# Kernel tuning notes

Measured on AMD Instinct MI355X. Metric: run time of the kernel, lower is better.

The kernel has to match this reference:

```python
import jax, jax.numpy as jnp
import numpy as np

# dims
N, M, L, E = 50000, 1024, 3, 200000      # tgt nodes, src nodes, subtokens/node, edges
HID, EMB, VOCAB = 512, 256, 512
N_SLT, N_SRT = 4, 5                       # SLT edge types (messages), SRT edge types (output head)
W_SCALE = 0.02


def setup_inputs() -> dict:
    key = jax.random.key(0)
    ks = jax.random.split(key, 20)
    inp = {
        "tgt_x": jax.random.randint(ks[0], (N, L), 0, VOCAB),
        "x": jax.random.normal(ks[1], (M, HID), jnp.float32),
        "tgt_edge_index": jax.random.randint(ks[2], (2, E), 0, N),
        "tgt_edge_type": jax.random.randint(ks[3], (E,), 0, N_SLT),
        "embed_table": jax.random.normal(ks[4], (VOCAB, EMB), jnp.float32) * W_SCALE,
        # GCN layer 1 (called twice in the original forward) and layer 3 params
        "W_h1": jax.random.normal(ks[5], (EMB, EMB), jnp.float32) * W_SCALE,
        "W_rel1": jax.random.normal(ks[6], (N_SLT, EMB, EMB), jnp.float32) * W_SCALE,
        "W_src1": jax.random.normal(ks[7], (HID, EMB), jnp.float32) * W_SCALE,
        "W_h3": jax.random.normal(ks[8], (EMB, EMB), jnp.float32) * W_SCALE,
        "W_rel3": jax.random.normal(ks[9], (N_SLT, EMB, EMB), jnp.float32) * W_SCALE,
        "W_src3": jax.random.normal(ks[10], (HID, EMB), jnp.float32) * W_SCALE,
        # output heads
        "Wz": jax.random.normal(ks[11], (EMB, VOCAB), jnp.float32) * W_SCALE,
        "bz": jnp.zeros((VOCAB,), jnp.float32),
        "Wg": jax.random.normal(ks[12], (2 * EMB, N_SRT), jnp.float32) * W_SCALE,
        "bg": jnp.zeros((N_SRT,), jnp.float32),
    }
    return inp


def _gcn_layer(x_src, h, edge_index, edge_type, W_h, W_rel, W_src):
    """Relational GCN decoder layer with cross-attention to encoder nodes."""
    k = x_src @ W_src                                   # [M, EMB]
    attn = jax.nn.softmax(h @ k.T / jnp.sqrt(jnp.float32(EMB)), axis=1)  # [N, M]
    ctx = attn @ k                                      # [N, EMB]
    # per-edge-type transform first ([N, T, EMB]), then gather per edge
    h_t = jnp.einsum('nd,tdf->ntf', h, W_rel)           # [N, N_SLT, EMB]
    src, tgt = edge_index[0], edge_index[1]
    msg = h_t[src, edge_type]                           # [E, EMB] gather
    agg = jax.ops.segment_sum(msg, tgt, num_segments=h.shape[0])  # [N, EMB]
    return jax.nn.relu(h @ W_h + agg + ctx)


def reference(tgt_x, x, tgt_edge_index, tgt_edge_type, embed_table,
              W_h1, W_rel1, W_src1, W_h3, W_rel3, W_src3, Wz, bz, Wg, bg):
    # embedding + reduction over subtokens
    h = embed_table[tgt_x].sum(axis=1)                  # [N, EMB]
    # original code calls gcn1 twice, then gcn3 (gcn2 unused in training path)
    h = _gcn_layer(x, h, tgt_edge_index, tgt_edge_type, W_h1, W_rel1, W_src1)
    h = _gcn_layer(x, h, tgt_edge_index, tgt_edge_type, W_h1, W_rel1, W_src1)
    h = _gcn_layer(x, h, tgt_edge_index, tgt_edge_type, W_h3, W_rel3, W_src3)
    # node head
    node_pred = jax.nn.log_softmax(h @ Wz + bz, axis=1)  # [N, VOCAB]
    # edge head: gather [2,E,EMB] -> permute -> [E, 2*EMB]
    ef = h[tgt_edge_index]                               # [2, E, EMB]
    ef = jnp.transpose(ef, (1, 0, 2)).reshape(E, 2 * EMB)
    edge_pred = jax.nn.log_softmax(ef @ Wg + bg, axis=1)  # [E, N_SRT]
    return node_pred, edge_pred
```

## Files before the change

### kernel.cpp

```cpp
#include <hip/hip_runtime.h>
#include <hip/hip_bf16.h>
#include <cstdint>

#define N_NODES 50000
#define M_SRC   1024
#define E_EDGES 200000
#define EMB     256
#define HIDN    512
#define VOCABSZ 512

typedef __attribute__((ext_vector_type(8))) short bf16x8;
typedef __attribute__((ext_vector_type(4))) short bf16x4;
typedef __attribute__((ext_vector_type(4))) float f32x4;

__device__ inline short f2b(float f) {
    __hip_bfloat16 b = __float2bfloat16(f);
    return *reinterpret_cast<short*>(&b);
}
__device__ inline float b2f(short s) {
    __hip_bfloat16 b = *reinterpret_cast<__hip_bfloat16*>(&s);
    return __bfloat162float(b);
}

__device__ inline void gload16(const void* g, void* l) {
    __builtin_amdgcn_global_load_lds(
        (const __attribute__((address_space(1))) unsigned int*)g,
        (__attribute__((address_space(3))) unsigned int*)l,
        16, 0, 0);
}

__device__ inline void tr_read2(unsigned addr, bf16x4& lo, bf16x4& hi) {
    asm volatile("ds_read_b64_tr_b16 %0, %2\n\tds_read_b64_tr_b16 %1, %2 offset:512"
                 : "=&v"(lo), "=&v"(hi) : "v"(addr));
}

__global__ void embed_kernel(const int* __restrict__ tgt_x,
                             const float* __restrict__ table,
                             short* __restrict__ h)
{
    int n = blockIdx.x, d = threadIdx.x;
    const int* tx = tgt_x + (size_t)n * 3;
    float s = table[(size_t)tx[0] * EMB + d]
            + table[(size_t)tx[1] * EMB + d]
            + table[(size_t)tx[2] * EMB + d];
    h[(size_t)n * EMB + d] = f2b(s);
}

__global__ void convert_kernel(const float* __restrict__ in, short* __restrict__ out, int n)
{
    int i = blockIdx.x * 256 + threadIdx.x;
    if (i * 4 < n) {
        float4 v = *(const float4*)&in[i * 4];
        short4 o;
        o.x = f2b(v.x); o.y = f2b(v.y); o.z = f2b(v.z); o.w = f2b(v.w);
        *(short4*)&out[i * 4] = o;
    }
}

template<typename TIN>
__global__ void transpose_kernel(const TIN* __restrict__ in, short* __restrict__ out, int R, int C)
{
    __shared__ float t[32][33];
    int tx = threadIdx.x & 31, ty = threadIdx.x >> 5;
    int r0 = blockIdx.y * 32, c0 = blockIdx.x * 32;
#pragma unroll
    for (int i = 0; i < 4; i++) {
        int r = ty + i * 8;
        TIN v = in[(size_t)(r0 + r) * C + c0 + tx];
        if constexpr (sizeof(TIN) == 4) t[r][tx] = v;
        else                            t[r][tx] = b2f(v);
    }
    __syncthreads();
#pragma unroll
    for (int i = 0; i < 4; i++) {
        int r = ty + i * 8;
        out[(size_t)(c0 + r) * R + r0 + tx] = f2b(t[tx][r]);
    }
}

__global__ void transposeW_kernel(const float* __restrict__ Wh1, const float* __restrict__ Wh3,
                                  const float* __restrict__ Wr1, const float* __restrict__ Wr3,
                                  short* __restrict__ WhT1, short* __restrict__ WhT3,
                                  short* __restrict__ WrT1, short* __restrict__ WrT3)
{
    __shared__ float t[32][33];
    const int z = blockIdx.z;
    const float* in; short* outp;
    if (z == 0)      { in = Wh1;                               outp = WhT1; }
    else if (z == 1) { in = Wh3;                               outp = WhT3; }
    else if (z < 6)  { in = Wr1 + (size_t)(z - 2) * EMB * EMB; outp = WrT1 + (size_t)(z - 2) * EMB * EMB; }
    else             { in = Wr3 + (size_t)(z - 6) * EMB * EMB; outp = WrT3 + (size_t)(z - 6) * EMB * EMB; }
    int tx = threadIdx.x & 31, ty = threadIdx.x >> 5;
    int r0 = blockIdx.y * 32, c0 = blockIdx.x * 32;
#pragma unroll
    for (int i = 0; i < 4; i++) {
        int r = ty + i * 8;
        t[r][tx] = in[(size_t)(r0 + r) * EMB + c0 + tx];
    }
    __syncthreads();
#pragma unroll
    for (int i = 0; i < 4; i++) {
        int r = ty + i * 8;
        outp[(size_t)(c0 + r) * EMB + r0 + tx] = f2b(t[tx][r]);
    }
}

template<int MODE>
__global__ __launch_bounds__(256) void mgemm(
    const short* __restrict__ A, const short* __restrict__ BT,
    void* __restrict__ outp, const float* __restrict__ aux,
    const float* __restrict__ bias, int NR, int K, int J)
{
    __shared__ short As[128 * 40];
    __shared__ short Bs[128 * 40];
    const int tid  = threadIdx.x;
    const int n0   = blockIdx.x * 128;
    const int j0   = blockIdx.y * 128;
    const int lane = tid & 63, wid = tid >> 6;
    const int wr   = wid >> 1, wc = wid & 1;

    f32x4 acc[4][4];
#pragma unroll
    for (int m = 0; m < 4; m++)
#pragma unroll
        for (int n = 0; n < 4; n++) acc[m][n] = (f32x4){0.f, 0.f, 0.f, 0.f};

    for (int kt = 0; kt < K; kt += 32) {
#pragma unroll
        for (int r = 0; r < 2; r++) {
            int idx = tid + r * 256;
            int row = idx >> 2, ko = (idx & 3) * 8;
            int n = n0 + row;
            bf16x8 av = {0, 0, 0, 0, 0, 0, 0, 0};
            if (n < NR) av = *(const bf16x8*)&A[(size_t)n * K + kt + ko];
            *(bf16x8*)&As[row * 40 + ko] = av;
            *(bf16x8*)&Bs[row * 40 + ko] = *(const bf16x8*)&BT[(size_t)(j0 + row) * K + kt + ko];
        }
        __syncthreads();
        bf16x8 af[4], bfr[4];
#pragma unroll
        for (int m = 0; m < 4; m++)
            af[m] = *(const bf16x8*)&As[(wr * 64 + m * 16 + (lane & 15)) * 40 + (lane >> 4) * 8];
#pragma unroll
        for (int n = 0; n < 4; n++)
            bfr[n] = *(const bf16x8*)&Bs[(wc * 64 + n * 16 + (lane & 15)) * 40 + (lane >> 4) * 8];
#pragma unroll
        for (int m = 0; m < 4; m++)
#pragma unroll
            for (int n = 0; n < 4; n++)
                acc[m][n] = __builtin_amdgcn_mfma_f32_16x16x32_bf16(af[m], bfr[n], acc[m][n], 0, 0, 0);
        __syncthreads();
    }

#pragma unroll
    for (int m = 0; m < 4; m++) {
        int rbase = wr * 64 + m * 16 + ((lane >> 4) * 4);
#pragma unroll
        for (int r = 0; r < 4; r++) {
            int n_g = n0 + rbase + r;
            if (n_g >= NR) continue;
#pragma unroll
            for (int nn = 0; nn < 4; nn++) {
                int j_g = j0 + wc * 64 + nn * 16 + (lane & 15);
                float v = acc[m][nn][r];
                if constexpr (MODE == 0) {
                    ((short*)outp)[(size_t)n_g * J + j_g] = f2b(v);
                } else {
                    float a = aux[(size_t)n_g * J + j_g];
                    ((short*)outp)[(size_t)n_g * J + j_g] = f2b(fmaxf(v + a, 0.f));
                }
            }
        }
    }
}

__global__ __launch_bounds__(256, 2) void attn_flash(
    const short* __restrict__ h, const short* __restrict__ kb,
    float* __restrict__ C, int NR)
{
    __shared__ short ks[2][32 * 256];
    __shared__ short Ps[64 * 36];

    const int tid = threadIdx.x;
    const int lane = tid & 63, wv = tid >> 6;
    const int l4 = lane >> 4, l15 = lane & 15;
    const int n0 = blockIdx.x * 64;
    const int hrow = wv * 16 + l15;

    auto LOFF = [](int key, int d8) {
        return (d8 & 1) * 8 + (key & 3) * 16 + ((key >> 3) & 3) * 64
             + ((key >> 2) & 1) * 256 + (d8 >> 1) * 512;
    };
    int keyq[4], d8q[4];
#pragma unroll
    for (int q = 0; q < 4; q++) {
        int ci = wv * 64 + lane + q * 256;
        d8q[q]  = (ci & 1) | ((ci >> 6) << 1);
        keyq[q] = ((ci >> 1) & 3) | (((ci >> 5) & 1) << 2) | (((ci >> 3) & 3) << 3);
    }

    bf16x8 hreg[8];
    {
        int n = n0 + hrow;
        const short* hp = &h[(size_t)(n < NR ? n : 0) * 256 + l4 * 8];
#pragma unroll
        for (int kst = 0; kst < 8; kst++) hreg[kst] = *(const bf16x8*)&hp[kst * 32];
        if (n >= NR) {
#pragma unroll
            for (int kst = 0; kst < 8; kst++) hreg[kst] = (bf16x8){0, 0, 0, 0, 0, 0, 0, 0};
        }
    }

#pragma unroll
    for (int q = 0; q < 4; q++)
        gload16(&kb[(size_t)keyq[q] * 256 + d8q[q] * 8], &ks[0][q * 2048 + wv * 512]);
    __syncthreads();

    const unsigned ksbase = (unsigned)(uintptr_t)&ks[0][0];
    const unsigned trlane = 2u * (unsigned)(l15 + l4 * 64);

    f32x4 oacc[16];
#pragma unroll
    for (int mm = 0; mm < 16; mm++) oacc[mm] = (f32x4){0.f, 0.f, 0.f, 0.f};
    float lsum = 0.f;

    for (int c = 0; c < 32; c++) {
        const int cur = c & 1;
        if (c + 1 < 32) {
            const short* kbn = kb + (size_t)(c + 1) * 32 * 256;
#pragma unroll
            for (int q = 0; q < 4; q++)
                gload16(&kbn[(size_t)keyq[q] * 256 + d8q[q] * 8], &ks[cur ^ 1][q * 2048 + wv * 512]);
        }

        f32x4 sacc[2];
        sacc[0] = (f32x4){0.f, 0.f, 0.f, 0.f};
        sacc[1] = (f32x4){0.f, 0.f, 0.f, 0.f};
        __builtin_amdgcn_s_setprio(1);
#pragma unroll
        for (int kst = 0; kst < 8; kst++) {
#pragma unroll
            for (int m = 0; m < 2; m++) {
                int krow = m * 16 + l15;
                bf16x8 afk = *(const bf16x8*)&ks[cur][LOFF(krow, kst * 4 + l4)];
                sacc[m] = __builtin_amdgcn_mfma_f32_16x16x32_bf16(afk, hreg[kst], sacc[m], 0, 0, 0);
            }
        }
        __builtin_amdgcn_s_setprio(0);
        float psum = 0.f;
#pragma unroll
        for (int m = 0; m < 2; m++) {
            float p0 = __expf(sacc[m][0] * 0.0625f);
            float p1 = __expf(sacc[m][1] * 0.0625f);
            float p2 = __expf(sacc[m][2] * 0.0625f);
            float p3 = __expf(sacc[m][3] * 0.0625f);
            psum += (p0 + p1) + (p2 + p3);
            short4 pk;
            pk.x = f2b(p0); pk.y = f2b(p1); pk.z = f2b(p2); pk.w = f2b(p3);
            *(short4*)&Ps[hrow * 36 + m * 16 + l4 * 4] = pk;
        }
        psum += __shfl_xor(psum, 16);
        psum += __shfl_xor(psum, 32);
        lsum += psum;

        bf16x8 bf2 = *(const bf16x8*)&Ps[(wv * 16 + l15) * 36 + l4 * 8];
        unsigned trb = ksbase + (unsigned)(cur * 16384) + trlane;
#pragma unroll
        for (int g = 0; g < 2; g++) {
            bf16x4 lo[8], hi[8];
#pragma unroll
            for (int q = 0; q < 8; q++)
                tr_read2(trb + (unsigned)((g * 8 + q) * 1024), lo[q], hi[q]);
            asm volatile("s_waitcnt lgkmcnt(0)" ::: "memory");
            __builtin_amdgcn_sched_barrier(0);
            __builtin_amdgcn_s_setprio(1);
#pragma unroll
            for (int q = 0; q < 8; q++) {
                bf16x8 af2;
#pragma unroll
                for (int t2 = 0; t2 < 4; t2++) { af2[t2] = lo[q][t2]; af2[t2 + 4] = hi[q][t2]; }
                oacc[g * 8 + q] = __builtin_amdgcn_mfma_f32_16x16x32_bf16(af2, bf2, oacc[g * 8 + q], 0, 0, 0);
            }
            __builtin_amdgcn_s_setprio(0);
        }

        __syncthreads();
    }

    float li = 1.0f / lsum;
    int hr = n0 + hrow;
    if (hr < NR) {
#pragma unroll
        for (int mm = 0; mm < 16; mm++) {
            float4 v;
            v.x = oacc[mm][0] * li;
            v.y = oacc[mm][1] * li;
            v.z = oacc[mm][2] * li;
            v.w = oacc[mm][3] * li;
            *(float4*)&C[(size_t)hr * 256 + mm * 16 + l4 * 4] = v;
        }
    }
}

__global__ void hist_kernel(const int* __restrict__ ei, int* __restrict__ deg)
{
    int e = blockIdx.x * 256 + threadIdx.x;
    if (e < E_EDGES) atomicAdd(&deg[ei[E_EDGES + e]], 1);
}

__global__ void scan1_kernel(const int* __restrict__ deg, int* __restrict__ incl,
                             int* __restrict__ bsum)
{
    __shared__ int s[256];
    int i = blockIdx.x * 256 + threadIdx.x;
    int v = (i < N_NODES) ? deg[i] : 0;
    s[threadIdx.x] = v;
    __syncthreads();
#pragma unroll
    for (int off = 1; off < 256; off <<= 1) {
        int t = (threadIdx.x >= off) ? s[threadIdx.x - off] : 0;
        __syncthreads();
        s[threadIdx.x] += t;
        __syncthreads();
    }
    if (i < N_NODES) incl[i] = s[threadIdx.x];
    if (threadIdx.x == 255) bsum[blockIdx.x] = s[255];
}

__global__ void scan2_kernel(int* __restrict__ bsum, int nb)
{
    __shared__ int s[256];
    int v = (threadIdx.x < nb) ? bsum[threadIdx.x] : 0;
    s[threadIdx.x] = v;
    __syncthreads();
#pragma unroll
    for (int off = 1; off < 256; off <<= 1) {
        int t = (threadIdx.x >= off) ? s[threadIdx.x - off] : 0;
        __syncthreads();
        s[threadIdx.x] += t;
        __syncthreads();
    }
    if (threadIdx.x < nb) bsum[threadIdx.x] = s[threadIdx.x];
}

__global__ void scan3_kernel(const int* __restrict__ deg, const int* __restrict__ incl,
                             const int* __restrict__ bsum, int* __restrict__ row_ptr,
                             int* __restrict__ cursor)
{
    int i = blockIdx.x * 256 + threadIdx.x;
    if (i >= N_NODES) return;
    int pref = (blockIdx.x > 0) ? bsum[blockIdx.x - 1] : 0;
    int start = pref + incl[i] - deg[i];
    row_ptr[i] = start;
    cursor[i]  = start;
    if (i == N_NODES - 1) row_ptr[N_NODES] = pref + incl[i];
}

__global__ void fill_kernel(const int* __restrict__ ei, const int* __restrict__ et,
                            int* __restrict__ cursor, int* __restrict__ eidx)
{
    int e = blockIdx.x * 256 + threadIdx.x;
    if (e >= E_EDGES) return;
    int tg = ei[E_EDGES + e];
    int slot = atomicAdd(&cursor[tg], 1);
    eidx[slot] = ei[e] | (et[e] << 16);
}

__global__ void agg_kernel(const int* __restrict__ row_ptr, const int* __restrict__ eidx,
                           const short* __restrict__ G, float* __restrict__ C)
{
    int w = (blockIdx.x * 256 + threadIdx.x) >> 6;
    if (w >= N_NODES) return;
    int lane = threadIdx.x & 63;
    int s0 = row_ptr[w], s1 = row_ptr[w + 1];
    float a0 = 0.f, a1 = 0.f, a2 = 0.f, a3 = 0.f;
    for (int i = s0; i < s1; i++) {
        int p = eidx[i];
        int s = p & 0xFFFF, t = p >> 16;
        short4 g = *(const short4*)&G[(size_t)s * 1024 + t * 256 + lane * 4];
        a0 += b2f(g.x); a1 += b2f(g.y); a2 += b2f(g.z); a3 += b2f(g.w);
    }
    float4 c = *(float4*)&C[(size_t)w * EMB + lane * 4];
    c.x += a0; c.y += a1; c.z += a2; c.w += a3;
    *(float4*)&C[(size_t)w * EMB + lane * 4] = c;
}

__global__ __launch_bounds__(512, 2) void head_kernel(
    const short* __restrict__ hmat, const short* __restrict__ WzT,
    const float* __restrict__ bz, float* __restrict__ out, int NR)
{
    __shared__ short hs[64 * 256];
    __shared__ float redm[64 * 8];
    __shared__ float reds[64 * 8];

    const int tid = threadIdx.x;
    const int lane = tid & 63, wv = tid >> 6;
    const int l4 = lane >> 4, l15 = lane & 15;
    const int n0 = blockIdx.x * 64;

#pragma unroll
    for (int i = 0; i < 4; i++) {
        int idx = tid + i * 512;
        int row = idx >> 5, kg = idx & 31;
        bf16x8 v = {0, 0, 0, 0, 0, 0, 0, 0};
        if (n0 + row < NR) v = *(const bf16x8*)&hmat[(size_t)(n0 + row) * 256 + kg * 8];
        *(bf16x8*)&hs[(row * 256 + kg * 8) ^ ((row & 7) << 3)] = v;
    }
    __syncthreads();

    f32x4 acc[4][4];
#pragma unroll
    for (int m = 0; m < 4; m++)
#pragma unroll
        for (int n = 0; n < 4; n++) acc[m][n] = (f32x4){0.f, 0.f, 0.f, 0.f};

#pragma unroll
    for (int kt = 0; kt < 256; kt += 32) {
        bf16x8 af[4], bfr[4];
#pragma unroll
        for (int m = 0; m < 4; m++) {
            int row = m * 16 + l15;
            af[m] = *(const bf16x8*)&hs[(row * 256 + kt + l4 * 8) ^ ((row & 7) << 3)];
        }
#pragma unroll
        for (int n = 0; n < 4; n++) {
            int col = wv * 64 + n * 16 + l15;
            bfr[n] = *(const bf16x8*)&WzT[(size_t)col * 256 + kt + l4 * 8];
        }
#pragma unroll
        for (int m = 0; m < 4; m++)
#pragma unroll
            for (int n = 0; n < 4; n++)
                acc[m][n] = __builtin_amdgcn_mfma_f32_16x16x32_bf16(af[m], bfr[n], acc[m][n], 0, 0, 0);
    }

    float bcol[4];
#pragma unroll
    for (int n = 0; n < 4; n++) bcol[n] = bz[wv * 64 + n * 16 + l15];
#pragma unroll
    for (int m = 0; m < 4; m++)
#pragma unroll
        for (int n = 0; n < 4; n++)
#pragma unroll
            for (int r = 0; r < 4; r++) acc[m][n][r] += bcol[n];

    float lg[4][4];
#pragma unroll
    for (int m = 0; m < 4; m++)
#pragma unroll
        for (int r = 0; r < 4; r++) {
            float v = fmaxf(fmaxf(acc[m][0][r], acc[m][1][r]), fmaxf(acc[m][2][r], acc[m][3][r]));
            v = fmaxf(v, __shfl_xor(v, 1));
            v = fmaxf(v, __shfl_xor(v, 2));
            v = fmaxf(v, __shfl_xor(v, 4));
            v = fmaxf(v, __shfl_xor(v, 8));
            if (l15 == 0) redm[(m * 16 + l4 * 4 + r) * 8 + wv] = v;
        }
    __syncthreads();
#pragma unroll
    for (int m = 0; m < 4; m++)
#pragma unroll
        for (int r = 0; r < 4; r++) {
            int row = m * 16 + l4 * 4 + r;
            float v = redm[row * 8 + 0];
#pragma unroll
            for (int w = 1; w < 8; w++) v = fmaxf(v, redm[row * 8 + w]);
            lg[m][r] = v;
        }
#pragma unroll
    for (int m = 0; m < 4; m++)
#pragma unroll
        for (int r = 0; r < 4; r++) {
            float gm = lg[m][r];
            float s = __expf(acc[m][0][r] - gm) + __expf(acc[m][1][r] - gm)
                    + __expf(acc[m][2][r] - gm) + __expf(acc[m][3][r] - gm);
            s += __shfl_xor(s, 1);
            s += __shfl_xor(s, 2);
            s += __shfl_xor(s, 4);
            s += __shfl_xor(s, 8);
            if (l15 == 0) reds[(m * 16 + l4 * 4 + r) * 8 + wv] = s;
        }
    __syncthreads();
#pragma unroll
    for (int m = 0; m < 4; m++)
#pragma unroll
        for (int r = 0; r < 4; r++) {
            int row = m * 16 + l4 * 4 + r;
            float s = reds[row * 8 + 0];
#pragma unroll
            for (int w = 1; w < 8; w++) s += reds[row * 8 + w];
            lg[m][r] += __logf(s);
        }
#pragma unroll
    for (int m = 0; m < 4; m++)
#pragma unroll
        for (int r = 0; r < 4; r++) {
            int hr = n0 + m * 16 + l4 * 4 + r;
            if (hr >= NR) continue;
#pragma unroll
            for (int n = 0; n < 4; n++)
                out[(size_t)hr * VOCABSZ + wv * 64 + n * 16 + l15] = acc[m][n][r] - lg[m][r];
        }
}

__global__ __launch_bounds__(256) void nodeproj_kernel(
    const short* __restrict__ h, const float* __restrict__ Wg,
    float* __restrict__ eproj)
{
    int lane = threadIdx.x & 63;
    int gw   = (blockIdx.x * 256 + threadIdx.x) >> 6;
    int nw   = (gridDim.x * 256) >> 6;
    float ws[4][5], wt[4][5];
#pragma unroll
    for (int c = 0; c < 4; c++)
#pragma unroll
        for (int j = 0; j < 5; j++) {
            ws[c][j] = Wg[(size_t)(lane * 4 + c) * 5 + j];
            wt[c][j] = Wg[(size_t)(256 + lane * 4 + c) * 5 + j];
        }

    for (int n = gw; n < N_NODES; n += nw) {
        short4 hv = *(const short4*)&h[(size_t)n * EMB + lane * 4];
        float f[4] = { b2f(hv.x), b2f(hv.y), b2f(hv.z), b2f(hv.w) };
        float a[5] = {0, 0, 0, 0, 0}, b[5] = {0, 0, 0, 0, 0};
#pragma unroll
        for (int c = 0; c < 4; c++)
#pragma unroll
            for (int j = 0; j < 5; j++) {
                a[j] += f[c] * ws[c][j];
                b[j] += f[c] * wt[c][j];
            }
#pragma unroll
        for (int j = 0; j < 5; j++)
#pragma unroll
            for (int off = 32; off; off >>= 1) {
                a[j] += __shfl_xor(a[j], off);
                b[j] += __shfl_xor(b[j], off);
            }
        if (lane == 0) {
#pragma unroll
            for (int j = 0; j < 5; j++) {
                eproj[(size_t)n * 10 + j]     = a[j];
                eproj[(size_t)n * 10 + 5 + j] = b[j];
            }
        }
    }
}

__global__ void edge_lsm_kernel(const int* __restrict__ ei,
                                const float* __restrict__ eproj,
                                const float* __restrict__ bg,
                                float* __restrict__ out)
{
    int e = blockIdx.x * 256 + threadIdx.x;
    if (e >= E_EDGES) return;
    int s = ei[e], t = ei[E_EDGES + e];
    const float* ps = &eproj[(size_t)s * 10];
    const float* pt = &eproj[(size_t)t * 10 + 5];
    float z[5];
#pragma unroll
    for (int j = 0; j < 5; j++) z[j] = ps[j] + pt[j] + bg[j];
    float mm = fmaxf(fmaxf(fmaxf(z[0], z[1]), fmaxf(z[2], z[3])), z[4]);
    float ss = __expf(z[0] - mm) + __expf(z[1] - mm) + __expf(z[2] - mm)
             + __expf(z[3] - mm) + __expf(z[4] - mm);
    float lg = mm + __logf(ss);
    float* o = &out[(size_t)e * 5];
#pragma unroll
    for (int j = 0; j < 5; j++) o[j] = z[j] - lg;
}

extern "C" void kernel_launch(void* const* d_in, const int* in_sizes, int n_in,
                              void* d_out, int out_size, void* d_ws, size_t ws_size,
                              hipStream_t stream)
{
    const int*   tgt_x = (const int*)  d_in[0];
    const float* x     = (const float*)d_in[1];
    const int*   ei    = (const int*)  d_in[2];
    const int*   et    = (const int*)  d_in[3];
    const float* table = (const float*)d_in[4];
    const float* Wh1   = (const float*)d_in[5];
    const float* Wrel1 = (const float*)d_in[6];
    const float* Wsrc1 = (const float*)d_in[7];
    const float* Wh3   = (const float*)d_in[8];
    const float* Wrel3 = (const float*)d_in[9];
    const float* Wsrc3 = (const float*)d_in[10];
    const float* Wz    = (const float*)d_in[11];
    const float* bz    = (const float*)d_in[12];
    const float* Wg    = (const float*)d_in[13];
    const float* bg    = (const float*)d_in[14];
    float* out = (float*)d_out;

    short* h_a = (short*)d_ws;
    short* h_b = h_a + (size_t)N_NODES * EMB;
    float* C   = (float*)(h_b + (size_t)N_NODES * EMB);
    short* PG  = (short*)(C + (size_t)N_NODES * EMB);
    short* k1b = PG + (size_t)N_NODES * 1024;
    short* k3b = k1b + M_SRC * EMB;
    short* x_b = k3b + M_SRC * EMB;
    short* WsT1 = x_b + M_SRC * HIDN;
    short* WsT3 = WsT1 + EMB * HIDN;
    short* WhT1 = WsT3 + EMB * HIDN;
    short* WhT3 = WhT1 + EMB * EMB;
    short* WrT1 = WhT3 + EMB * EMB;
    short* WrT3 = WrT1 + 4 * EMB * EMB;
    short* WzT  = WrT3 + 4 * EMB * EMB;
    int* deg     = (int*)(WzT + VOCABSZ * EMB);
    int* incl    = deg + N_NODES;
    int* bsum    = incl + N_NODES;
    int* row_ptr = bsum + 256;
    int* cursor  = row_ptr + N_NODES + 1;
    int* eidx    = cursor + N_NODES;
    float* eproj = (float*)(eidx + E_EDGES);

    const int gN = (N_NODES + 127) / 128;
    const int gN64 = (N_NODES + 63) / 64;
    const int nb1 = (N_NODES + 255) / 256;

    hipMemsetAsync(deg, 0, N_NODES * sizeof(int), stream);
    hist_kernel<<<(E_EDGES + 255) / 256, 256, 0, stream>>>(ei, deg);
    scan1_kernel<<<nb1, 256, 0, stream>>>(deg, incl, bsum);
    scan2_kernel<<<1, 256, 0, stream>>>(bsum, nb1);
    scan3_kernel<<<nb1, 256, 0, stream>>>(deg, incl, bsum, row_ptr, cursor);
    fill_kernel<<<(E_EDGES + 255) / 256, 256, 0, stream>>>(ei, et, cursor, eidx);

    convert_kernel<<<(M_SRC * HIDN / 4 + 255) / 256, 256, 0, stream>>>(x, x_b, M_SRC * HIDN);
    transpose_kernel<float><<<dim3(EMB / 32, HIDN / 32), 256, 0, stream>>>(Wsrc1, WsT1, HIDN, EMB);
    transpose_kernel<float><<<dim3(EMB / 32, HIDN / 32), 256, 0, stream>>>(Wsrc3, WsT3, HIDN, EMB);
    transposeW_kernel<<<dim3(8, 8, 10), 256, 0, stream>>>(Wh1, Wh3, Wrel1, Wrel3,
                                                          WhT1, WhT3, WrT1, WrT3);
    transpose_kernel<float><<<dim3(VOCABSZ / 32, EMB / 32), 256, 0, stream>>>(Wz, WzT, EMB, VOCABSZ);

    mgemm<0><<<dim3(M_SRC / 128, EMB / 128), 256, 0, stream>>>(x_b, WsT1, k1b, nullptr, nullptr, M_SRC, HIDN, EMB);
    mgemm<0><<<dim3(M_SRC / 128, EMB / 128), 256, 0, stream>>>(x_b, WsT3, k3b, nullptr, nullptr, M_SRC, HIDN, EMB);

    embed_kernel<<<N_NODES, 256, 0, stream>>>(tgt_x, table, h_a);

    short* h_cur = h_a;
    short* h_nxt = h_b;
    for (int layer = 0; layer < 3; layer++) {
        const short* kb  = (layer < 2) ? k1b  : k3b;
        const short* WrT = (layer < 2) ? WrT1 : WrT3;
        const short* WhT = (layer < 2) ? WhT1 : WhT3;

        attn_flash<<<gN64, 256, 0, stream>>>(h_cur, kb, C, N_NODES);
        mgemm<0><<<dim3(gN, 8), 256, 0, stream>>>(h_cur, WrT, PG, nullptr, nullptr,
                                                  N_NODES, EMB, 4 * EMB);
        agg_kernel<<<(N_NODES + 3) / 4, 256, 0, stream>>>(row_ptr, eidx, PG, C);
        mgemm<3><<<dim3(gN, EMB / 128), 256, 0, stream>>>(h_cur, WhT, h_nxt, C, nullptr,
                                                          N_NODES, EMB, EMB);
        short* tmp = h_cur; h_cur = h_nxt; h_nxt = tmp;
    }

    head_kernel<<<gN64, 512, 0, stream>>>(h_cur, WzT, bz, out, N_NODES);

    nodeproj_kernel<<<2048, 256, 0, stream>>>(h_cur, Wg, eproj);
    edge_lsm_kernel<<<(E_EDGES + 255) / 256, 256, 0, stream>>>(ei, eproj, bg,
                                                               out + (size_t)N_NODES * VOCABSZ);
}
```

Baseline: 895.0 us.

## Aggregate raw features per edge type before transform; fuse into one wide GEMM

Reorders the relational message computation so that neighbor features are first summed per edge type (agg2_kernel), and the four relation transforms plus the self transform then run as a single K=1280 GEMM against a concatenated weight matrix. This removes the [N,1024] per-node transformed-feature GEMM output and its gather, and drops one GEMM launch per layer. The attention kernel is also retuned to 128 threads, with each wave handling two 16-row groups so it reuses loaded key fragments. Risks include bf16 rounding of the aggregated sums, the branchy per-type accumulation in the aggregation kernel, and a wide GEMM with a simple non-pipelined load loop.

```diff
diff --git a/kernel.cpp b/kernel.cpp
--- a/kernel.cpp
+++ b/kernel.cpp
@@ -8,6 +8,7 @@
 #define EMB     256
 #define HIDN    512
 #define VOCABSZ 512
+#define KW      1280
 
 typedef __attribute__((ext_vector_type(8))) short bf16x8;
 typedef __attribute__((ext_vector_type(4))) short bf16x4;
@@ -80,16 +81,15 @@
 
 __global__ void transposeW_kernel(const float* __restrict__ Wh1, const float* __restrict__ Wh3,
                                   const float* __restrict__ Wr1, const float* __restrict__ Wr3,
-                                  short* __restrict__ WhT1, short* __restrict__ WhT3,
-                                  short* __restrict__ WrT1, short* __restrict__ WrT3)
+                                  short* __restrict__ Wcat1, short* __restrict__ Wcat3)
 {
     __shared__ float t[32][33];
     const int z = blockIdx.z;
-    const float* in; short* outp;
-    if (z == 0)      { in = Wh1;                               outp = WhT1; }
-    else if (z == 1) { in = Wh3;                               outp = WhT3; }
-    else if (z < 6)  { in = Wr1 + (size_t)(z - 2) * EMB * EMB; outp = WrT1 + (size_t)(z - 2) * EMB * EMB; }
-    else             { in = Wr3 + (size_t)(z - 6) * EMB * EMB; outp = WrT3 + (size_t)(z - 6) * EMB * EMB; }
+    const float* in; short* outp; int coloff;
+    if (z == 0)      { in = Wh1;                               outp = Wcat1; coloff = 0; }
+    else if (z == 1) { in = Wh3;                               outp = Wcat3; coloff = 0; }
+    else if (z < 6)  { in = Wr1 + (size_t)(z - 2) * EMB * EMB; outp = Wcat1; coloff = 256 + (z - 2) * 256; }
+    else             { in = Wr3 + (size_t)(z - 6) * EMB * EMB; outp = Wcat3; coloff = 256 + (z - 6) * 256; }
     int tx = threadIdx.x & 31, ty = threadIdx.x >> 5;
     int r0 = blockIdx.y * 32, c0 = blockIdx.x * 32;
 #pragma unroll
@@ -101,7 +101,7 @@
 #pragma unroll
     for (int i = 0; i < 4; i++) {
         int r = ty + i * 8;
-        outp[(size_t)(c0 + r) * EMB + r0 + tx] = f2b(t[tx][r]);
+        outp[(size_t)(c0 + r) * KW + coloff + r0 + tx] = f2b(t[tx][r]);
     }
 }
 
@@ -162,19 +162,80 @@
 #pragma unroll
             for (int nn = 0; nn < 4; nn++) {
                 int j_g = j0 + wc * 64 + nn * 16 + (lane & 15);
-                float v = acc[m][nn][r];
-                if constexpr (MODE == 0) {
-                    ((short*)outp)[(size_t)n_g * J + j_g] = f2b(v);
-                } else {
-                    float a = aux[(size_t)n_g * J + j_g];
-                    ((short*)outp)[(size_t)n_g * J + j_g] = f2b(fmaxf(v + a, 0.f));
-                }
-            }
-        }
-    }
-}
-
-__global__ __launch_bounds__(256, 2) void attn_flash(
+                ((short*)outp)[(size_t)n_g * J + j_g] = f2b(acc[m][nn][r]);
+            }
+        }
+    }
+}
+
+__global__ __launch_bounds__(256) void mgemm_wide(
+    const short* __restrict__ A1, const short* __restrict__ A2,
+    const short* __restrict__ BT, short* __restrict__ outp,
+    const float* __restrict__ aux, int NR)
+{
+    __shared__ short As[128 * 40];
+    __shared__ short Bs[128 * 40];
+    const int tid  = threadIdx.x;
+    const int n0   = blockIdx.x * 128;
+    const int j0   = blockIdx.y * 128;
+    const int lane = tid & 63, wid = tid >> 6;
+    const int wr   = wid >> 1, wc = wid & 1;
+
+    f32x4 acc[4][4];
+#pragma unroll
+    for (int m = 0; m < 4; m++)
+#pragma unroll
+        for (int n = 0; n < 4; n++) acc[m][n] = (f32x4){0.f, 0.f, 0.f, 0.f};
+
+    for (int kt = 0; kt < KW; kt += 32) {
+#pragma unroll
+        for (int r = 0; r < 2; r++) {
+            int idx = tid + r * 256;
+            int row = idx >> 2, ko = (idx & 3) * 8;
+            int n = n0 + row;
+            bf16x8 av = {0, 0, 0, 0, 0, 0, 0, 0};
+            if (n < NR) {
+                const short* ap = (kt < 256) ? &A1[(size_t)n * 256 + kt + ko]
+                                             : &A2[(size_t)n * 1024 + (kt - 256) + ko];
+                av = *(const bf16x8*)ap;
+            }
+            *(bf16x8*)&As[row * 40 + ko] = av;
+            *(bf16x8*)&Bs[row * 40 + ko] = *(const bf16x8*)&BT[(size_t)(j0 + row) * KW + kt + ko];
+        }
+        __syncthreads();
+        bf16x8 af[4], bfr[4];
+#pragma unroll
+        for (int m = 0; m < 4; m++)
+            af[m] = *(const bf16x8*)&As[(wr * 64 + m * 16 + (lane & 15)) * 40 + (lane >> 4) * 8];
+#pragma unroll
+        for (int n = 0; n < 4; n++)
+            bfr[n] = *(const bf16x8*)&Bs[(wc * 64 + n * 16 + (lane & 15)) * 40 + (lane >> 4) * 8];
+#pragma unroll
+        for (int m = 0; m < 4; m++)
+#pragma unroll
+            for (int n = 0; n < 4; n++)
+                acc[m][n] = __builtin_amdgcn_mfma_f32_16x16x32_bf16(af[m], bfr[n], acc[m][n], 0, 0, 0);
+        __syncthreads();
+    }
+
+#pragma unroll
+    for (int m = 0; m < 4; m++) {
+        int rbase = wr * 64 + m * 16 + ((lane >> 4) * 4);
+#pragma unroll
+        for (int r = 0; r < 4; r++) {
+            int n_g = n0 + rbase + r;
+            if (n_g >= NR) continue;
+#pragma unroll
+            for (int nn = 0; nn < 4; nn++) {
+                int j_g = j0 + wc * 64 + nn * 16 + (lane & 15);
+                float v = acc[m][nn][r] + aux[(size_t)n_g * 256 + j_g];
+                outp[(size_t)n_g * 256 + j_g] = f2b(fmaxf(v, 0.f));
+            }
+        }
+    }
+}
+
+__global__ __launch_bounds__(128, 2) void attn_flash(
     const short* __restrict__ h, const short* __restrict__ kb,
     float* __restrict__ C, int NR)
 {
@@ -185,57 +246,64 @@
     const int lane = tid & 63, wv = tid >> 6;
     const int l4 = lane >> 4, l15 = lane & 15;
     const int n0 = blockIdx.x * 64;
-    const int hrow = wv * 16 + l15;
 
     auto LOFF = [](int key, int d8) {
         return (d8 & 1) * 8 + (key & 3) * 16 + ((key >> 3) & 3) * 64
              + ((key >> 2) & 1) * 256 + (d8 >> 1) * 512;
     };
-    int keyq[4], d8q[4];
-#pragma unroll
-    for (int q = 0; q < 4; q++) {
-        int ci = wv * 64 + lane + q * 256;
+    int keyq[8], d8q[8];
+#pragma unroll
+    for (int q = 0; q < 8; q++) {
+        int ci = wv * 64 + lane + q * 128;
         d8q[q]  = (ci & 1) | ((ci >> 6) << 1);
         keyq[q] = ((ci >> 1) & 3) | (((ci >> 5) & 1) << 2) | (((ci >> 3) & 3) << 3);
     }
 
-    bf16x8 hreg[8];
-    {
-        int n = n0 + hrow;
+    bf16x8 hreg[2][8];
+#pragma unroll
+    for (int rg = 0; rg < 2; rg++) {
+        int n = n0 + wv * 32 + rg * 16 + l15;
         const short* hp = &h[(size_t)(n < NR ? n : 0) * 256 + l4 * 8];
 #pragma unroll
-        for (int kst = 0; kst < 8; kst++) hreg[kst] = *(const bf16x8*)&hp[kst * 32];
+        for (int kst = 0; kst < 8; kst++) hreg[rg][kst] = *(const bf16x8*)&hp[kst * 32];
         if (n >= NR) {
 #pragma unroll
-            for (int kst = 0; kst < 8; kst++) hreg[kst] = (bf16x8){0, 0, 0, 0, 0, 0, 0, 0};
-        }
-    }
-
-#pragma unroll
-    for (int q = 0; q < 4; q++)
-        gload16(&kb[(size_t)keyq[q] * 256 + d8q[q] * 8], &ks[0][q * 2048 + wv * 512]);
+            for (int kst = 0; kst < 8; kst++) hreg[rg][kst] = (bf16x8){0, 0, 0, 0, 0, 0, 0, 0};
+        }
+    }
+
+#pragma unroll
+    for (int q = 0; q < 8; q++)
+        gload16(&kb[(size_t)keyq[q] * 256 + d8q[q] * 8],
+                (char*)&ks[0][0] + q * 2048 + wv * 1024);
     __syncthreads();
 
     const unsigned ksbase = (unsigned)(uintptr_t)&ks[0][0];
     const unsigned trlane = 2u * (unsigned)(l15 + l4 * 64);
 
-    f32x4 oacc[16];
-#pragma unroll
-    for (int mm = 0; mm < 16; mm++) oacc[mm] = (f32x4){0.f, 0.f, 0.f, 0.f};
-    float lsum = 0.f;
+    f32x4 oacc[2][16];
+#pragma unroll
+    for (int rg = 0; rg < 2; rg++)
+#pragma unroll
+        for (int mm = 0; mm < 16; mm++) oacc[rg][mm] = (f32x4){0.f, 0.f, 0.f, 0.f};
+    float lsum[2] = {0.f, 0.f};
 
     for (int c = 0; c < 32; c++) {
         const int cur = c & 1;
         if (c + 1 < 32) {
             const short* kbn = kb + (size_t)(c + 1) * 32 * 256;
 #pragma unroll
-            for (int q = 0; q < 4; q++)
-                gload16(&kbn[(size_t)keyq[q] * 256 + d8q[q] * 8], &ks[cur ^ 1][q * 2048 + wv * 512]);
-        }
-
-        f32x4 sacc[2];
-        sacc[0] = (f32x4){0.f, 0.f, 0.f, 0.f};
-        sacc[1] = (f32x4){0.f, 0.f, 0.f, 0.f};
+            for (int q = 0; q < 8; q++)
+                gload16(&kbn[(size_t)keyq[q] * 256 + d8q[q] * 8],
+                        (char*)&ks[cur ^ 1][0] + q * 2048 + wv * 1024);
+        }
+
+        f32x4 sacc[2][2];
+#pragma unroll
+        for (int rg = 0; rg < 2; rg++) {
+            sacc[rg][0] = (f32x4){0.f, 0.f, 0.f, 0.f};
+            sacc[rg][1] = (f32x4){0.f, 0.f, 0.f, 0.f};
+        }
         __builtin_amdgcn_s_setprio(1);
 #pragma unroll
         for (int kst = 0; kst < 8; kst++) {
@@ -243,27 +311,36 @@
             for (int m = 0; m < 2; m++) {
                 int krow = m * 16 + l15;
                 bf16x8 afk = *(const bf16x8*)&ks[cur][LOFF(krow, kst * 4 + l4)];
-                sacc[m] = __builtin_amdgcn_mfma_f32_16x16x32_bf16(afk, hreg[kst], sacc[m], 0, 0, 0);
+                sacc[0][m] = __builtin_amdgcn_mfma_f32_16x16x32_bf16(afk, hreg[0][kst], sacc[0][m], 0, 0, 0);
+                sacc[1][m] = __builtin_amdgcn_mfma_f32_16x16x32_bf16(afk, hreg[1][kst], sacc[1][m], 0, 0, 0);
             }
         }
         __builtin_amdgcn_s_setprio(0);
-        float psum = 0.f;
-#pragma unroll
-        for (int m = 0; m < 2; m++) {
-            float p0 = __expf(sacc[m][0] * 0.0625f);
-            float p1 = __expf(sacc[m][1] * 0.0625f);
-            float p2 = __expf(sacc[m][2] * 0.0625f);
-            float p3 = __expf(sacc[m][3] * 0.0625f);
-            psum += (p0 + p1) + (p2 + p3);
-            short4 pk;
-            pk.x = f2b(p0); pk.y = f2b(p1); pk.z = f2b(p2); pk.w = f2b(p3);
-            *(short4*)&Ps[hrow * 36 + m * 16 + l4 * 4] = pk;
-        }
-        psum += __shfl_xor(psum, 16);
-        psum += __shfl_xor(psum, 32);
-        lsum += psum;
-
-        bf16x8 bf2 = *(const bf16x8*)&Ps[(wv * 16 + l15) * 36 + l4 * 8];
+
+#pragma unroll
+        for (int rg = 0; rg < 2; rg++) {
+            int prow = wv * 32 + rg * 16 + l15;
+            float psum = 0.f;
+#pragma unroll
+            for (int m = 0; m < 2; m++) {
+                float p0 = __expf(sacc[rg][m][0] * 0.0625f);
+                float p1 = __expf(sacc[rg][m][1] * 0.0625f);
+                float p2 = __expf(sacc[rg][m][2] * 0.0625f);
+                float p3 = __expf(sacc[rg][m][3] * 0.0625f);
+                psum += (p0 + p1) + (p2 + p3);
+                short4 pk;
+                pk.x = f2b(p0); pk.y = f2b(p1); pk.z = f2b(p2); pk.w = f2b(p3);
+                *(short4*)&Ps[prow * 36 + m * 16 + l4 * 4] = pk;
+            }
+            psum += __shfl_xor(psum, 16);
+            psum += __shfl_xor(psum, 32);
+            lsum[rg] += psum;
+        }
+
+        bf16x8 bf2[2];
+#pragma unroll
+        for (int rg = 0; rg < 2; rg++)
+            bf2[rg] = *(const bf16x8*)&Ps[(wv * 32 + rg * 16 + l15) * 36 + l4 * 8];
         unsigned trb = ksbase + (unsigned)(cur * 16384) + trlane;
 #pragma unroll
         for (int g = 0; g < 2; g++) {
@@ -279,7 +356,8 @@
                 bf16x8 af2;
 #pragma unroll
                 for (int t2 = 0; t2 < 4; t2++) { af2[t2] = lo[q][t2]; af2[t2 + 4] = hi[q][t2]; }
-                oacc[g * 8 + q] = __builtin_amdgcn_mfma_f32_16x16x32_bf16(af2, bf2, oacc[g * 8 + q], 0, 0, 0);
+                oacc[0][g * 8 + q] = __builtin_amdgcn_mfma_f32_16x16x32_bf16(af2, bf2[0], oacc[0][g * 8 + q], 0, 0, 0);
+                oacc[1][g * 8 + q] = __builtin_amdgcn_mfma_f32_16x16x32_bf16(af2, bf2[1], oacc[1][g * 8 + q], 0, 0, 0);
             }
             __builtin_amdgcn_s_setprio(0);
         }
@@ -287,16 +365,18 @@
         __syncthreads();
     }
 
-    float li = 1.0f / lsum;
-    int hr = n0 + hrow;
-    if (hr < NR) {
+#pragma unroll
+    for (int rg = 0; rg < 2; rg++) {
+        float li = 1.0f / lsum[rg];
+        int hr = n0 + wv * 32 + rg * 16 + l15;
+        if (hr >= NR) continue;
 #pragma unroll
         for (int mm = 0; mm < 16; mm++) {
             float4 v;
-            v.x = oacc[mm][0] * li;
-            v.y = oacc[mm][1] * li;
-            v.z = oacc[mm][2] * li;
-            v.w = oacc[mm][3] * li;
+            v.x = oacc[rg][mm][0] * li;
+            v.y = oacc[rg][mm][1] * li;
+            v.z = oacc[rg][mm][2] * li;
+            v.w = oacc[rg][mm][3] * li;
             *(float4*)&C[(size_t)hr * 256 + mm * 16 + l4 * 4] = v;
         }
     }
@@ -366,23 +446,33 @@
     eidx[slot] = ei[e] | (et[e] << 16);
 }
 
-__global__ void agg_kernel(const int* __restrict__ row_ptr, const int* __restrict__ eidx,
-                           const short* __restrict__ G, float* __restrict__ C)
+__global__ void agg2_kernel(const int* __restrict__ row_ptr, const int* __restrict__ eidx,
+                            const short* __restrict__ h, short* __restrict__ Bagg)
 {
     int w = (blockIdx.x * 256 + threadIdx.x) >> 6;
     if (w >= N_NODES) return;
     int lane = threadIdx.x & 63;
     int s0 = row_ptr[w], s1 = row_ptr[w + 1];
-    float a0 = 0.f, a1 = 0.f, a2 = 0.f, a3 = 0.f;
+    float a0[4] = {0, 0, 0, 0}, a1[4] = {0, 0, 0, 0}, a2[4] = {0, 0, 0, 0}, a3[4] = {0, 0, 0, 0};
     for (int i = s0; i < s1; i++) {
         int p = eidx[i];
         int s = p & 0xFFFF, t = p >> 16;
-        short4 g = *(const short4*)&G[(size_t)s * 1024 + t * 256 + lane * 4];
-        a0 += b2f(g.x); a1 += b2f(g.y); a2 += b2f(g.z); a3 += b2f(g.w);
-    }
-    float4 c = *(float4*)&C[(size_t)w * EMB + lane * 4];
-    c.x += a0; c.y += a1; c.z += a2; c.w += a3;
-    *(float4*)&C[(size_t)w * EMB + lane * 4] = c;
+        short4 g = *(const short4*)&h[(size_t)s * EMB + lane * 4];
+        float f0 = b2f(g.x), f1 = b2f(g.y), f2 = b2f(g.z), f3 = b2f(g.w);
+        if (t == 0)      { a0[0] += f0; a0[1] += f1; a0[2] += f2; a0[3] += f3; }
+        else if (t == 1) { a1[0] += f0; a1[1] += f1; a1[2] += f2; a1[3] += f3; }
+        else if (t == 2) { a2[0] += f0; a2[1] += f1; a2[2] += f2; a2[3] += f3; }
+        else             { a3[0] += f0; a3[1] += f1; a3[2] += f2; a3[3] += f3; }
+    }
+    short4 o;
+    o.x = f2b(a0[0]); o.y = f2b(a0[1]); o.z = f2b(a0[2]); o.w = f2b(a0[3]);
+    *(short4*)&Bagg[(size_t)w * 1024 + 0 * 256 + lane * 4] = o;
+    o.x = f2b(a1[0]); o.y = f2b(a1[1]); o.z = f2b(a1[2]); o.w = f2b(a1[3]);
+    *(short4*)&Bagg[(size_t)w * 1024 + 1 * 256 + lane * 4] = o;
+    o.x = f2b(a2[0]); o.y = f2b(a2[1]); o.z = f2b(a2[2]); o.w = f2b(a2[3]);
+    *(short4*)&Bagg[(size_t)w * 1024 + 2 * 256 + lane * 4] = o;
+    o.x = f2b(a3[0]); o.y = f2b(a3[1]); o.z = f2b(a3[2]); o.w = f2b(a3[3]);
+    *(short4*)&Bagg[(size_t)w * 1024 + 3 * 256 + lane * 4] = o;
 }
 
 __global__ __launch_bounds__(512, 2) void head_kernel(
@@ -593,17 +683,15 @@
     short* h_a = (short*)d_ws;
     short* h_b = h_a + (size_t)N_NODES * EMB;
     float* C   = (float*)(h_b + (size_t)N_NODES * EMB);
-    short* PG  = (short*)(C + (size_t)N_NODES * EMB);
-    short* k1b = PG + (size_t)N_NODES * 1024;
+    short* Bagg = (short*)(C + (size_t)N_NODES * EMB);
+    short* k1b = Bagg + (size_t)N_NODES * 1024;
     short* k3b = k1b + M_SRC * EMB;
     short* x_b = k3b + M_SRC * EMB;
     short* WsT1 = x_b + M_SRC * HIDN;
     short* WsT3 = WsT1 + EMB * HIDN;
-    short* WhT1 = WsT3 + EMB * HIDN;
-    short* WhT3 = WhT1 + EMB * EMB;
-    short* WrT1 = WhT3 + EMB * EMB;
-    short* WrT3 = WrT1 + 4 * EMB * EMB;
-    short* WzT  = WrT3 + 4 * EMB * EMB;
+    short* Wcat1 = WsT3 + EMB * HIDN;
+    short* Wcat3 = Wcat1 + EMB * KW;
+    short* WzT  = Wcat3 + EMB * KW;
     int* deg     = (int*)(WzT + VOCABSZ * EMB);
     int* incl    = deg + N_NODES;
     int* bsum    = incl + N_NODES;
@@ -626,8 +714,7 @@
     convert_kernel<<<(M_SRC * HIDN / 4 + 255) / 256, 256, 0, stream>>>(x, x_b, M_SRC * HIDN);
     transpose_kernel<float><<<dim3(EMB / 32, HIDN / 32), 256, 0, stream>>>(Wsrc1, WsT1, HIDN, EMB);
     transpose_kernel<float><<<dim3(EMB / 32, HIDN / 32), 256, 0, stream>>>(Wsrc3, WsT3, HIDN, EMB);
-    transposeW_kernel<<<dim3(8, 8, 10), 256, 0, stream>>>(Wh1, Wh3, Wrel1, Wrel3,
-                                                          WhT1, WhT3, WrT1, WrT3);
+    transposeW_kernel<<<dim3(8, 8, 10), 256, 0, stream>>>(Wh1, Wh3, Wrel1, Wrel3, Wcat1, Wcat3);
     transpose_kernel<float><<<dim3(VOCABSZ / 32, EMB / 32), 256, 0, stream>>>(Wz, WzT, EMB, VOCABSZ);
 
     mgemm<0><<<dim3(M_SRC / 128, EMB / 128), 256, 0, stream>>>(x_b, WsT1, k1b, nullptr, nullptr, M_SRC, HIDN, EMB);
@@ -638,16 +725,12 @@
     short* h_cur = h_a;
     short* h_nxt = h_b;
     for (int layer = 0; layer < 3; layer++) {
-        const short* kb  = (layer < 2) ? k1b  : k3b;
-        const short* WrT = (layer < 2) ? WrT1 : WrT3;
-        const short* WhT = (layer < 2) ? WhT1 : WhT3;
-
-        attn_flash<<<gN64, 256, 0, stream>>>(h_cur, kb, C, N_NODES);
-        mgemm<0><<<dim3(gN, 8), 256, 0, stream>>>(h_cur, WrT, PG, nullptr, nullptr,
-                                                  N_NODES, EMB, 4 * EMB);
-        agg_kernel<<<(N_NODES + 3) / 4, 256, 0, stream>>>(row_ptr, eidx, PG, C);
-        mgemm<3><<<dim3(gN, EMB / 128), 256, 0, stream>>>(h_cur, WhT, h_nxt, C, nullptr,
-                                                          N_NODES, EMB, EMB);
+        const short* kb   = (layer < 2) ? k1b   : k3b;
+        const short* Wcat = (layer < 2) ? Wcat1 : Wcat3;
+
+        attn_flash<<<gN64, 128, 0, stream>>>(h_cur, kb, C, N_NODES);
+        agg2_kernel<<<(N_NODES + 3) / 4, 256, 0, stream>>>(row_ptr, eidx, h_cur, Bagg);
+        mgemm_wide<<<dim3(gN, 2), 256, 0, stream>>>(h_cur, Bagg, Wcat, h_nxt, C, N_NODES);
         short* tmp = h_cur; h_cur = h_nxt; h_nxt = tmp;
     }
 
```

Measured after the change: 840.3 us. -6.1%, faster.
